# Optimization experiments

Hardware: AMD Instinct MI355X
Metric: run time of the kernel (lower is better)

Reference implementation:

```python
import jax, jax.numpy as jnp
import numpy as np

# ---- config (matches init_kwargs) ----
M, N, D = 8, 512, 243            # meshes, neurons per mesh, input dim
E_RATIO = 0.8
NE = int(N * E_RATIO)            # 409 excitatory
NI = N - NE                      # 103 inhibitory
TICKS = 16
BATCH = 512
BITS = 4
WSCALE = 8.0
VTH, VRESET = 1.0, 0.0
TAU_E, TAU_I, DT = 2.0, 1.5, 1.0
BETA = 10.0                      # fast-sigmoid surrogate slope
INPUT_SCALE = 1.0


def fake_quant(w):
    """Quantization-aware fake quant with straight-through estimator."""
    step = WSCALE / (2 ** (BITS - 1))          # 1.0 for 4-bit, scale 8
    q = jnp.clip(jnp.round(w / step), -(2 ** (BITS - 1)), 2 ** (BITS - 1) - 1) * step
    return w + jax.lax.stop_gradient(q - w)


@jax.custom_vjp
def spike(u):
    return (u >= 0.0).astype(u.dtype)

def _spike_fwd(u):
    return spike(u), u

def _spike_bwd(u, g):
    # fast-sigmoid surrogate gradient
    return (g * BETA / (1.0 + BETA * jnp.abs(u)) ** 2,)

spike.defvjp(_spike_fwd, _spike_bwd)


def setup_inputs() -> dict:
    key = jax.random.key(0)
    ks = jax.random.split(key, 8)

    def sparse_w(k, shape, density, std, zero_diag=False):
        km, kw = jax.random.split(k)
        mask = (jax.random.uniform(km, shape) < density).astype(jnp.float32)
        if zero_diag:
            mask = mask * (1.0 - jnp.eye(shape[-1], dtype=jnp.float32))
        return jax.random.normal(kw, shape) * std * mask

    x = jax.random.normal(ks[0], (BATCH, D), dtype=jnp.float32)
    W_in = jax.random.normal(ks[1], (M, N, D)) * 0.8      # per-mesh input projection [out,in]
    b_in = jax.random.normal(ks[2], (M, N)) * 0.05
    W_inter = sparse_w(ks[3], (M, N, NE), 0.3, 0.8)        # inter-mesh: E of mesh m -> mesh m+1
    W_EE = sparse_w(ks[4], (M, NE, NE), 0.5, 0.8, True)
    W_EI = sparse_w(ks[5], (M, NI, NE), 0.6, 0.8)
    W_IE = sparse_w(ks[6], (M, NE, NI), 0.8, 0.8)
    W_II = sparse_w(ks[7], (M, NI, NI), 0.7, 0.8, True)
    return dict(x=x, W_in=W_in, b_in=b_in, W_inter=W_inter,
                W_EE=W_EE, W_EI=W_EI, W_IE=W_IE, W_II=W_II)


def reference(x, W_in, b_in, W_inter, W_EE, W_EI, W_IE, W_II):
    B = x.shape[0]
    decay_E = 1.0 - DT / TAU_E
    decay_I = 1.0 - DT / TAU_I

    # quantize weights once (constant across ticks)
    qW_in, qW_inter = fake_quant(W_in), fake_quant(W_inter)
    qW_EE, qW_EI = fake_quant(W_EE), fake_quant(W_EI)
    qW_IE, qW_II = fake_quant(W_IE), fake_quant(W_II)

    # external input projection, same every tick: [M, B, N]
    ext_proj = jnp.einsum('bd,mnd->mbn', x * INPUT_SCALE, qW_in) + b_in[:, None, :]

    def tick(carry, _):
        e, i, vE, vI, acc = carry          # e:[M,B,NE] i:[M,B,NI]
        # inter-mesh: mesh m receives inter_connections[m-1](e_prev[m-1])
        inter = jnp.einsum('mbe,mne->mbn', e, qW_inter)
        ext = ext_proj + jnp.roll(inter, 1, axis=0)
        cE = ext[:, :, :NE] \
            + jnp.einsum('mbe,mfe->mbf', e, qW_EE) \
            + jnp.einsum('mbi,mfi->mbf', i, qW_IE)
        cI = ext[:, :, NE:] \
            + jnp.einsum('mbe,mfe->mbf', e, qW_EI) \
            + jnp.einsum('mbi,mfi->mbf', i, qW_II)
        # LIF: leaky decay + input, threshold, hard reset
        vE = vE * decay_E + cE * DT
        vI = vI * decay_I + cI * DT
        sE = spike(vE - VTH)
        sI = spike(vI - VTH)
        vE = sE * VRESET + (1.0 - sE) * vE
        vI = sI * VRESET + (1.0 - sI) * vI
        acc = acc + jnp.concatenate([sE, sI], axis=-1)
        return (sE, sI, vE, vI, acc), None

    z = jnp.zeros
    carry0 = (z((M, B, NE)), z((M, B, NI)), z((M, B, NE)), z((M, B, NI)), z((M, B, N)))
    (eF, iF, vEF, vIF, acc), _ = jax.lax.scan(tick, carry0, None, length=TICKS)
    # accumulator laid out mesh-major: [B, M*N]
    return jnp.transpose(acc, (1, 0, 2)).reshape(B, M * N)
```

## Files before the change

kernel.cpp:

```cpp
#include <hip/hip_runtime.h>
#include <hip/hip_bf16.h>

#define Mm 8
#define Nn 512
#define NEe 409
#define NIi 103
#define Bb 512
#define Dd 243
#define Tt 16
#define SPB 96
#define SPTICK (Mm * Bb * SPB)
#define WCROW 1152
#define DEC_I 0.33333334f
#define NBLK 256
#define FLAGSTRIDE 16
#define SPINMAX 1000000L
#define ABROW 176
#define ZSPAN_U32 1581056

typedef int v4i __attribute__((ext_vector_type(4)));

__device__ __forceinline__ float quantf(float w) {
    float q = rintf(w);
    return fminf(fmaxf(q, -8.0f), 7.0f);
}

__device__ __forceinline__ v4i unpack16(unsigned int dl, unsigned int dh, bool qhi, int qsh) {
    unsigned int d = qhi ? dh : dl;
    v4i r;
    r[0] = (int)((((d >> qsh) & 0xFu) * 0x00204081u) & 0x01010101u);
    r[1] = (int)((((d >> (qsh + 4)) & 0xFu) * 0x00204081u) & 0x01010101u);
    r[2] = (int)((((d >> (qsh + 8)) & 0xFu) * 0x00204081u) & 0x01010101u);
    r[3] = (int)((((d >> (qsh + 12)) & 0xFu) * 0x00204081u) & 0x01010101u);
    return r;
}

__global__ void k_pack(const float* __restrict__ Wint, const float* __restrict__ WEE,
                       const float* __restrict__ WEI, const float* __restrict__ WIE,
                       const float* __restrict__ WII, signed char* __restrict__ Wc,
                       unsigned* __restrict__ spz) {
    int gid = blockIdx.x * 256 + threadIdx.x;
#pragma unroll
    for (int z = 0; z < 2; ++z) {
        int i = gid + z * 1179648;
        if (i < ZSPAN_U32) spz[i] = 0u;
    }
    int q = gid;
    if (q >= (Mm * Nn * WCROW) / 4) return;
    int k0 = (q * 4) % WCROW;
    int n  = ((q * 4) / WCROW) & (Nn - 1);
    int m  = (q * 4) / (WCROW * Nn);
    char out4[4];
#pragma unroll
    for (int j = 0; j < 4; ++j) {
        int k = k0 + j;
        float w = 0.0f;
        if (k < 512) {
            if (k < NEe) w = Wint[((((m + 7) & 7) * Nn) + n) * NEe + k];
        } else if (k < 1024) {
            int jj = k - 512;
            if (jj < NEe) w = (n < NEe) ? WEE[((m * NEe) + n) * NEe + jj]
                                        : WEI[((m * NIi) + (n - NEe)) * NEe + jj];
        } else {
            int jj = k - 1049;
            if (jj >= 0 && jj < NIi) w = (n < NEe) ? WIE[((m * NEe) + n) * NIi + jj]
                                        : WII[((m * NIi) + (n - NEe)) * NIi + jj];
        }
        out4[j] = (signed char)(int)quantf(w);
    }
    *(int*)&Wc[q * 4] = *(int*)out4;
}

__global__ void __launch_bounds__(512, 2)
k_ticks(const signed char* __restrict__ Wc,
        unsigned char* __restrict__ Sp,
        const float* __restrict__ x,
        const float* __restrict__ Win,
        const float* __restrict__ bin,
        float* __restrict__ out,
        int* __restrict__ flags) {
    __shared__ __align__(16) signed char sB[128 * WCROW];
    __shared__ __align__(16) unsigned char sAb[64 * ABROW];

    const int wg = blockIdx.x;
    const int m  = wg & 7;
    const int bt = (wg >> 3) & 7;
    const int nt = wg >> 6;
    const int b0 = bt * 64;
    const int n0 = nt * 128;
    const int pm = (m + 7) & 7;

    const int tid  = threadIdx.x;
    const int w    = tid >> 6;
    const int lane = tid & 63;
    const int bh   = w & 1;
    const int nh   = w >> 1;
    const int quad = lane >> 4;
    const int li   = lane & 15;

    int waitIdx = 0;
    if (tid < 8) {
        int mm = (tid < 4) ? pm : m;
        waitIdx = (((tid & 3) << 6) | (bt << 3) | mm) * FLAGSTRIDE;
    }

    float decs[2]; int nels[2];
    int styp[2], soff[2];
#pragma unroll
    for (int tn = 0; tn < 2; ++tn) {
        int n = n0 + nh * 32 + tn * 16 + li;
        nels[tn] = n;
        decs[tn] = (n < NEe) ? 0.5f : DEC_I;
        int nb = n0 + nh * 32 + tn * 16;
        if (nb < 400)      { styp[tn] = 0; soff[tn] = nb >> 3; }
        else if (nb == 400){ styp[tn] = 2; soff[tn] = 50; }
        else               { styp[tn] = 1; soff[tn] = 64 + ((nb - 384) >> 3); }
    }
    const int bbase = b0 + bh * 32;

    {
        const int g   = tid >> 8;
        const int t8  = tid & 255;
        const int n0e = n0 + g * 64;
        float* xs  = (float*)sB + g * (2 * 64 * 68);
        float* wsm = xs + 64 * 68;
        const int etb4 = (t8 & 15) * 4;
        const int etn4 = (t8 >> 4) * 4;
        const int sr = t8 >> 2;
        const int sc = (t8 & 3) * 16;
        float c[4][4];
#pragma unroll
        for (int i = 0; i < 4; ++i)
#pragma unroll
            for (int j = 0; j < 4; ++j) c[i][j] = 0.0f;

        for (int d0 = 0; d0 < Dd; d0 += 64) {
#pragma unroll
            for (int j = 0; j < 16; ++j) {
                int d = d0 + sc + j;
                float xv = 0.0f, wv = 0.0f;
                if (d < Dd) {
                    xv = x[(b0 + sr) * Dd + d];
                    wv = quantf(Win[((m * Nn) + n0e + sr) * Dd + d]);
                }
                xs[(sc + j) * 68 + sr] = xv;
                wsm[(sc + j) * 68 + sr] = wv;
            }
            __syncthreads();
            const int dmax = min(64, Dd - d0);
            for (int d = 0; d < dmax; ++d) {
                float4 av = *(const float4*)&xs[d * 68 + etb4];
                float4 wv = *(const float4*)&wsm[d * 68 + etn4];
                float a[4] = {av.x, av.y, av.z, av.w};
                float wq[4] = {wv.x, wv.y, wv.z, wv.w};
#pragma unroll
                for (int i = 0; i < 4; ++i)
#pragma unroll
                    for (int j = 0; j < 4; ++j)
                        c[i][j] = fmaf(a[i], wq[j], c[i][j]);
            }
            __syncthreads();
        }
        float* extbuf = (float*)sB;
#pragma unroll
        for (int i = 0; i < 4; ++i)
#pragma unroll
            for (int j = 0; j < 4; ++j)
                extbuf[(etb4 + i) * 128 + g * 64 + etn4 + j] =
                    __fadd_rn(c[i][j], bin[m * Nn + n0e + etn4 + j]);
        __syncthreads();
    }

    float extr[2][2][4];
#pragma unroll
    for (int tb = 0; tb < 2; ++tb)
#pragma unroll
        for (int tn = 0; tn < 2; ++tn)
#pragma unroll
            for (int r = 0; r < 4; ++r)
                extr[tb][tn][r] = ((const float*)sB)[(bh * 32 + tb * 16 + quad * 4 + r) * 128
                                                     + (nels[tn] - n0)];
    __syncthreads();

    const signed char* WcBase = Wc + (size_t)(m * Nn + n0) * WCROW;
#pragma unroll
    for (int j = 0; j < 18; ++j) {
        int task = tid + j * 512;
        int row = task / 72, gg = task % 72;
        v4i v = *(const v4i*)(WcBase + (size_t)row * WCROW + gg * 16);
        int gs = (gg < 64) ? ((gg & 48) | ((gg ^ row) & 15))
                           : (64 + ((gg ^ row) & 7));
        *(v4i*)&sB[row * WCROW + gs * 16] = v;
    }
    if (tid < 384) {
        int row = tid / 6, z = tid - (tid / 6) * 6;
        int s = (z < 3) ? (13 + z) : (26 + z);
        *(unsigned*)&sAb[row * ABROW + s * 4] = 0u;
    }
    __syncthreads();

    float vmem[2][2][4];
    int cnt[2][2];
#pragma unroll
    for (int tb = 0; tb < 2; ++tb)
#pragma unroll
        for (int tn = 0; tn < 2; ++tn) {
            cnt[tb][tn] = 0;
#pragma unroll
            for (int r = 0; r < 4; ++r) vmem[tb][tn][r] = 0.0f;
        }

    const bool qhi = (quad >= 2);
    const int qsh = (quad & 1) << 4;
    const int r0base = (bh * 32 + li) * ABROW;
    const int r1base = (bh * 32 + 16 + li) * ABROW;

    for (int t = 0; t < Tt; ++t) {
        float c[2][2][4];

        if (t == 0) {
#pragma unroll
            for (int tb = 0; tb < 2; ++tb)
#pragma unroll
                for (int tn = 0; tn < 2; ++tn)
#pragma unroll
                    for (int r = 0; r < 4; ++r)
                        c[tb][tn][r] = __fadd_rn(__fadd_rn(__fadd_rn(extr[tb][tn][r], 0.0f), 0.0f), 0.0f);
        } else {
            if (tid < 8) {
                long spin = 0;
                while (__hip_atomic_load(&flags[waitIdx],
                                         __ATOMIC_RELAXED, __HIP_MEMORY_SCOPE_AGENT) < t) {
                    __builtin_amdgcn_s_sleep(2);
                    if (++spin > SPINMAX) break;
                }
            }
            __syncthreads();

            const unsigned char* SR = Sp + (size_t)(t - 1) * SPTICK;
            const unsigned char* PrevRow = SR + (size_t)(pm * Bb + b0) * SPB;
            const unsigned char* OwnRow  = SR + (size_t)(m  * Bb + b0) * SPB;
#pragma unroll
            for (int j = 0; j < 3; ++j) {
                int task = tid + j * 512;
                if (task < 1152) {
                    int row = task / 18, s = task % 18;
                    const unsigned char* src;
                    int dstoff;
                    if (s < 8)       { src = PrevRow + (size_t)row * SPB + s * 8;            dstoff = s * 8; }
                    else if (s < 16) { src = OwnRow  + (size_t)row * SPB + (s - 8) * 8;      dstoff = s * 8; }
                    else             { src = OwnRow  + (size_t)row * SPB + 64 + (s - 16) * 8; dstoff = 128 + (s - 16) * 8; }
                    unsigned long long vb = __hip_atomic_load((const unsigned long long*)src,
                                               __ATOMIC_RELAXED, __HIP_MEMORY_SCOPE_AGENT);
                    *(unsigned long long*)&sAb[row * ABROW + dstoff] = vb;
                }
            }
            __syncthreads();

            v4i acc[2][2];
#pragma unroll
            for (int tb = 0; tb < 2; ++tb)
#pragma unroll
                for (int tn = 0; tn < 2; ++tn) acc[tb][tn] = (v4i){0, 0, 0, 0};

#pragma unroll
            for (int ch = 0; ch < 4; ++ch) {
                const int cb = ch << 8;
                v4i a0lo = *(const v4i*)&sAb[r0base + (cb >> 3)];
                v4i a0hi = *(const v4i*)&sAb[r0base + (cb >> 3) + 16];
                v4i a1lo = *(const v4i*)&sAb[r1base + (cb >> 3)];
                v4i a1hi = *(const v4i*)&sAb[r1base + (cb >> 3) + 16];
#pragma unroll
                for (int ks = 0; ks < 256; ks += 64) {
                    v4i s0 = (ks < 128) ? a0lo : a0hi;
                    v4i s1 = (ks < 128) ? a1lo : a1hi;
                    const int D0 = ((ks >> 6) & 1) ? 2 : 0;
                    v4i af0 = unpack16((unsigned int)s0[D0], (unsigned int)s0[D0 + 1], qhi, qsh);
                    v4i af1 = unpack16((unsigned int)s1[D0], (unsigned int)s1[D0 + 1], qhi, qsh);
                    const int gs = (cb >> 4) + ((((ks >> 4) + quad) ^ li) & 15);
#pragma unroll
                    for (int tn = 0; tn < 2; ++tn) {
                        const v4i bfr = *(const v4i*)&sB[(nh * 32 + tn * 16 + li) * WCROW + gs * 16];
                        acc[0][tn] = __builtin_amdgcn_mfma_i32_16x16x64_i8(af0, bfr, acc[0][tn], 0, 0, 0);
                        acc[1][tn] = __builtin_amdgcn_mfma_i32_16x16x64_i8(af1, bfr, acc[1][tn], 0, 0, 0);
                    }
                }
                if (ch == 1) {
#pragma unroll
                    for (int tb = 0; tb < 2; ++tb)
#pragma unroll
                        for (int tn = 0; tn < 2; ++tn) {
#pragma unroll
                            for (int r = 0; r < 4; ++r)
                                c[tb][tn][r] = __fadd_rn(extr[tb][tn][r], (float)acc[tb][tn][r]);
                            acc[tb][tn] = (v4i){0, 0, 0, 0};
                        }
                } else if (ch == 3) {
#pragma unroll
                    for (int tb = 0; tb < 2; ++tb)
#pragma unroll
                        for (int tn = 0; tn < 2; ++tn) {
#pragma unroll
                            for (int r = 0; r < 4; ++r)
                                c[tb][tn][r] = __fadd_rn(c[tb][tn][r], (float)acc[tb][tn][r]);
                            acc[tb][tn] = (v4i){0, 0, 0, 0};
                        }
                }
            }
            {
                v4i e0 = *(const v4i*)&sAb[r0base + 128];
                v4i e1 = *(const v4i*)&sAb[r1base + 128];
#pragma unroll
                for (int ks = 0; ks < 128; ks += 64) {
                    const int D0 = (ks >> 6) ? 2 : 0;
                    v4i af0 = unpack16((unsigned int)e0[D0], (unsigned int)e0[D0 + 1], qhi, qsh);
                    v4i af1 = unpack16((unsigned int)e1[D0], (unsigned int)e1[D0 + 1], qhi, qsh);
                    const int gs = 64 + ((((ks >> 4) + quad) ^ li) & 7);
#pragma unroll
                    for (int tn = 0; tn < 2; ++tn) {
                        const v4i bfr = *(const v4i*)&sB[(nh * 32 + tn * 16 + li) * WCROW + gs * 16];
                        acc[0][tn] = __builtin_amdgcn_mfma_i32_16x16x64_i8(af0, bfr, acc[0][tn], 0, 0, 0);
                        acc[1][tn] = __builtin_amdgcn_mfma_i32_16x16x64_i8(af1, bfr, acc[1][tn], 0, 0, 0);
                    }
                }
            }
#pragma unroll
            for (int tb = 0; tb < 2; ++tb)
#pragma unroll
                for (int tn = 0; tn < 2; ++tn)
#pragma unroll
                    for (int r = 0; r < 4; ++r)
                        c[tb][tn][r] = __fadd_rn(c[tb][tn][r], (float)acc[tb][tn][r]);
        }

        int snow[2][2] = {{0, 0}, {0, 0}};
#pragma unroll
        for (int tb = 0; tb < 2; ++tb)
#pragma unroll
            for (int tn = 0; tn < 2; ++tn)
#pragma unroll
                for (int r = 0; r < 4; ++r) {
                    float vn = __fadd_rn(__fmul_rn(vmem[tb][tn][r], decs[tn]), c[tb][tn][r]);
                    int s = (vn >= 1.0f) ? 1 : 0;
                    vmem[tb][tn][r] = s ? 0.0f : vn;
                    cnt[tb][tn] += s << (r * 8);
                    snow[tb][tn] |= s << r;
                }

        if (t < Tt - 1) {
            unsigned char* SW = Sp + (size_t)t * SPTICK;
#pragma unroll
            for (int tb = 0; tb < 2; ++tb)
#pragma unroll
                for (int tn = 0; tn < 2; ++tn)
#pragma unroll
                    for (int r = 0; r < 4; ++r) {
                        unsigned long long mk = __ballot((snow[tb][tn] >> r) & 1);
                        if (li == 0) {
                            unsigned short v = (unsigned short)(mk >> (unsigned)(quad << 4));
                            int row = bbase + tb * 16 + quad * 4 + r;
                            unsigned char* rb = SW + (size_t)(m * Bb + row) * SPB;
                            if (styp[tn] != 2) {
                                __hip_atomic_store((unsigned short*)(rb + soff[tn]), v,
                                                   __ATOMIC_RELAXED, __HIP_MEMORY_SCOPE_AGENT);
                            } else {
                                __hip_atomic_store((unsigned short*)(rb + 50),
                                                   (unsigned short)(v & 0x01FF),
                                                   __ATOMIC_RELAXED, __HIP_MEMORY_SCOPE_AGENT);
                                __hip_atomic_store((unsigned short*)(rb + 66),
                                                   (unsigned short)(v & 0xFE00),
                                                   __ATOMIC_RELAXED, __HIP_MEMORY_SCOPE_AGENT);
                            }
                        }
                    }
            __syncthreads();
            if (tid == 0)
                __hip_atomic_store(&flags[wg * FLAGSTRIDE], t + 1,
                                   __ATOMIC_RELAXED, __HIP_MEMORY_SCOPE_AGENT);
        }
    }

#pragma unroll
    for (int tb = 0; tb < 2; ++tb)
#pragma unroll
        for (int tn = 0; tn < 2; ++tn)
#pragma unroll
            for (int r = 0; r < 4; ++r) {
                int b = bbase + tb * 16 + quad * 4 + r;
                out[(size_t)b * (Mm * Nn) + m * Nn + nels[tn]] =
                    (float)((cnt[tb][tn] >> (r * 8)) & 0xff);
            }
}

extern "C" void kernel_launch(void* const* d_in, const int* in_sizes, int n_in,
                              void* d_out, int out_size, void* d_ws, size_t ws_size,
                              hipStream_t stream) {
    const float* x    = (const float*)d_in[0];
    const float* Win  = (const float*)d_in[1];
    const float* bin  = (const float*)d_in[2];
    const float* Wint = (const float*)d_in[3];
    const float* WEE  = (const float*)d_in[4];
    const float* WEI  = (const float*)d_in[5];
    const float* WIE  = (const float*)d_in[6];
    const float* WII  = (const float*)d_in[7];
    float* out = (float*)d_out;

    char* ws = (char*)d_ws;
    signed char* Wc   = (signed char*)ws;
    unsigned char* Sp = (unsigned char*)(ws + 4718592);
    int* flags = (int*)(ws + 4718592 + 16 * SPTICK);

    k_pack<<<(Mm * Nn * WCROW / 4 + 255) / 256, 256, 0, stream>>>(Wint, WEE, WEI, WIE, WII, Wc,
                                                                  (unsigned*)Sp);
    k_ticks<<<NBLK, 512, 0, stream>>>(Wc, Sp, x, Win, bin, out, flags);
}
```

Baseline: 197.0 us.

## Halve neuron tile per block and stream weights through double-buffered LDS per tick

Workgroups now cover 64 neurons instead of 128, which doubles the grid to 512 blocks of 256 threads. The full weight slab is no longer kept resident in LDS. Each tick it is streamed from global memory in 256-column chunks through a double-buffered LDS stage, so LDS use drops enough to raise occupancy and spread the recurrent work over more blocks. The cost is that weights are re-read from global/L2 on every tick, there are extra barriers per chunk, and each block now waits on twice as many inter-block flags in the persistent spin-wait scheme.

```diff
diff --git a/kernel.cpp b/kernel.cpp
--- a/kernel.cpp
+++ b/kernel.cpp
@@ -12,7 +12,7 @@
 #define SPTICK (Mm * Bb * SPB)
 #define WCROW 1152
 #define DEC_I 0.33333334f
-#define NBLK 256
+#define NBLK 512
 #define FLAGSTRIDE 16
 #define SPINMAX 1000000L
 #define ABROW 176
@@ -71,7 +71,7 @@
     *(int*)&Wc[q * 4] = *(int*)out4;
 }
 
-__global__ void __launch_bounds__(512, 2)
+__global__ void __launch_bounds__(256, 2)
 k_ticks(const signed char* __restrict__ Wc,
         unsigned char* __restrict__ Sp,
         const float* __restrict__ x,
@@ -79,15 +79,16 @@
         const float* __restrict__ bin,
         float* __restrict__ out,
         int* __restrict__ flags) {
-    __shared__ __align__(16) signed char sB[128 * WCROW];
-    __shared__ __align__(16) unsigned char sAb[64 * ABROW];
+    __shared__ __align__(16) char arena[44032];
+    signed char (*sBst)[64][256] = (signed char (*)[64][256])arena;
+    unsigned char* sAb = (unsigned char*)(arena + 32768);
 
     const int wg = blockIdx.x;
     const int m  = wg & 7;
     const int bt = (wg >> 3) & 7;
     const int nt = wg >> 6;
     const int b0 = bt * 64;
-    const int n0 = nt * 128;
+    const int n0 = nt * 64;
     const int pm = (m + 7) & 7;
 
     const int tid  = threadIdx.x;
@@ -99,9 +100,9 @@
     const int li   = lane & 15;
 
     int waitIdx = 0;
-    if (tid < 8) {
-        int mm = (tid < 4) ? pm : m;
-        waitIdx = (((tid & 3) << 6) | (bt << 3) | mm) * FLAGSTRIDE;
+    if (tid < 16) {
+        int mm = (tid < 8) ? pm : m;
+        waitIdx = (((tid & 7) << 6) | (bt << 3) | mm) * FLAGSTRIDE;
     }
 
     float decs[2]; int nels[2];
@@ -119,11 +120,9 @@
     const int bbase = b0 + bh * 32;
 
     {
-        const int g   = tid >> 8;
-        const int t8  = tid & 255;
-        const int n0e = n0 + g * 64;
-        float* xs  = (float*)sB + g * (2 * 64 * 68);
-        float* wsm = xs + 64 * 68;
+        float* xs  = (float*)arena;
+        float* wsm = (float*)arena + 64 * 68;
+        const int t8 = tid;
         const int etb4 = (t8 & 15) * 4;
         const int etn4 = (t8 >> 4) * 4;
         const int sr = t8 >> 2;
@@ -141,7 +140,7 @@
                 float xv = 0.0f, wv = 0.0f;
                 if (d < Dd) {
                     xv = x[(b0 + sr) * Dd + d];
-                    wv = quantf(Win[((m * Nn) + n0e + sr) * Dd + d]);
+                    wv = quantf(Win[((m * Nn) + n0 + sr) * Dd + d]);
                 }
                 xs[(sc + j) * 68 + sr] = xv;
                 wsm[(sc + j) * 68 + sr] = wv;
@@ -161,13 +160,13 @@
             }
             __syncthreads();
         }
-        float* extbuf = (float*)sB;
+        float* extbuf = (float*)arena;
 #pragma unroll
         for (int i = 0; i < 4; ++i)
 #pragma unroll
             for (int j = 0; j < 4; ++j)
-                extbuf[(etb4 + i) * 128 + g * 64 + etn4 + j] =
-                    __fadd_rn(c[i][j], bin[m * Nn + n0e + etn4 + j]);
+                extbuf[(etb4 + i) * 64 + etn4 + j] =
+                    __fadd_rn(c[i][j], bin[m * Nn + n0 + etn4 + j]);
         __syncthreads();
     }
 
@@ -178,26 +177,27 @@
         for (int tn = 0; tn < 2; ++tn)
 #pragma unroll
             for (int r = 0; r < 4; ++r)
-                extr[tb][tn][r] = ((const float*)sB)[(bh * 32 + tb * 16 + quad * 4 + r) * 128
-                                                     + (nels[tn] - n0)];
+                extr[tb][tn][r] = ((const float*)arena)[(bh * 32 + tb * 16 + quad * 4 + r) * 64
+                                                        + (nels[tn] - n0)];
     __syncthreads();
 
-    const signed char* WcBase = Wc + (size_t)(m * Nn + n0) * WCROW;
-#pragma unroll
-    for (int j = 0; j < 18; ++j) {
-        int task = tid + j * 512;
-        int row = task / 72, gg = task % 72;
-        v4i v = *(const v4i*)(WcBase + (size_t)row * WCROW + gg * 16);
-        int gs = (gg < 64) ? ((gg & 48) | ((gg ^ row) & 15))
-                           : (64 + ((gg ^ row) & 7));
-        *(v4i*)&sB[row * WCROW + gs * 16] = v;
-    }
-    if (tid < 384) {
-        int row = tid / 6, z = tid - (tid / 6) * 6;
+    for (int idx = tid; idx < 384; idx += 256) {
+        int row = idx / 6, z = idx - (idx / 6) * 6;
         int s = (z < 3) ? (13 + z) : (26 + z);
         *(unsigned*)&sAb[row * ABROW + s * 4] = 0u;
     }
     __syncthreads();
+
+    int rowB[4], gcolB[4], scolB[4];
+#pragma unroll
+    for (int j = 0; j < 4; ++j) {
+        int ch = tid + j * 256;
+        rowB[j]  = ch >> 4;
+        int cnk  = ch & 15;
+        gcolB[j] = cnk * 16;
+        scolB[j] = (cnk ^ (rowB[j] & 15)) * 16;
+    }
+    const signed char* WcBase = Wc + (size_t)(m * Nn + n0) * WCROW;
 
     float vmem[2][2][4];
     int cnt[2][2];
@@ -214,6 +214,7 @@
     const int qsh = (quad & 1) << 4;
     const int r0base = (bh * 32 + li) * ABROW;
     const int r1base = (bh * 32 + 16 + li) * ABROW;
+    const int bRow0 = nh * 32 + li;
 
     for (int t = 0; t < Tt; ++t) {
         float c[2][2][4];
@@ -227,7 +228,7 @@
                     for (int r = 0; r < 4; ++r)
                         c[tb][tn][r] = __fadd_rn(__fadd_rn(__fadd_rn(extr[tb][tn][r], 0.0f), 0.0f), 0.0f);
         } else {
-            if (tid < 8) {
+            if (tid < 16) {
                 long spin = 0;
                 while (__hip_atomic_load(&flags[waitIdx],
                                          __ATOMIC_RELAXED, __HIP_MEMORY_SCOPE_AGENT) < t) {
@@ -241,8 +242,8 @@
             const unsigned char* PrevRow = SR + (size_t)(pm * Bb + b0) * SPB;
             const unsigned char* OwnRow  = SR + (size_t)(m  * Bb + b0) * SPB;
 #pragma unroll
-            for (int j = 0; j < 3; ++j) {
-                int task = tid + j * 512;
+            for (int j = 0; j < 5; ++j) {
+                int task = tid + j * 256;
                 if (task < 1152) {
                     int row = task / 18, s = task % 18;
                     const unsigned char* src;
@@ -255,6 +256,10 @@
                     *(unsigned long long*)&sAb[row * ABROW + dstoff] = vb;
                 }
             }
+#pragma unroll
+            for (int j = 0; j < 4; ++j)
+                *(v4i*)&sBst[0][rowB[j]][scolB[j]] =
+                    *(const v4i*)(WcBase + (size_t)rowB[j] * WCROW + gcolB[j]);
             __syncthreads();
 
             v4i acc[2][2];
@@ -263,9 +268,18 @@
 #pragma unroll
                 for (int tn = 0; tn < 2; ++tn) acc[tb][tn] = (v4i){0, 0, 0, 0};
 
-#pragma unroll
-            for (int ch = 0; ch < 4; ++ch) {
-                const int cb = ch << 8;
+            for (int it = 0; it < 4; ++it) {
+                const int buf = it & 1;
+                const int k0 = (it + 1) * 256;
+                const int kw = (it == 3) ? 128 : 256;
+                v4i nB[4]; bool ldB[4];
+#pragma unroll
+                for (int j = 0; j < 4; ++j) {
+                    ldB[j] = (gcolB[j] < kw);
+                    if (ldB[j])
+                        nB[j] = *(const v4i*)(WcBase + (size_t)rowB[j] * WCROW + k0 + gcolB[j]);
+                }
+                const int cb = it << 8;
                 v4i a0lo = *(const v4i*)&sAb[r0base + (cb >> 3)];
                 v4i a0hi = *(const v4i*)&sAb[r0base + (cb >> 3) + 16];
                 v4i a1lo = *(const v4i*)&sAb[r1base + (cb >> 3)];
@@ -277,15 +291,20 @@
                     const int D0 = ((ks >> 6) & 1) ? 2 : 0;
                     v4i af0 = unpack16((unsigned int)s0[D0], (unsigned int)s0[D0 + 1], qhi, qsh);
                     v4i af1 = unpack16((unsigned int)s1[D0], (unsigned int)s1[D0 + 1], qhi, qsh);
-                    const int gs = (cb >> 4) + ((((ks >> 4) + quad) ^ li) & 15);
+                    const int col = ((((ks >> 4) + quad) ^ li) & 15) * 16;
 #pragma unroll
                     for (int tn = 0; tn < 2; ++tn) {
-                        const v4i bfr = *(const v4i*)&sB[(nh * 32 + tn * 16 + li) * WCROW + gs * 16];
+                        const v4i bfr = *(const v4i*)&sBst[buf][bRow0 + tn * 16][col];
                         acc[0][tn] = __builtin_amdgcn_mfma_i32_16x16x64_i8(af0, bfr, acc[0][tn], 0, 0, 0);
                         acc[1][tn] = __builtin_amdgcn_mfma_i32_16x16x64_i8(af1, bfr, acc[1][tn], 0, 0, 0);
                     }
                 }
-                if (ch == 1) {
+                const int nb2 = buf ^ 1;
+#pragma unroll
+                for (int j = 0; j < 4; ++j)
+                    if (ldB[j]) *(v4i*)&sBst[nb2][rowB[j]][scolB[j]] = nB[j];
+                __syncthreads();
+                if (it == 1) {
 #pragma unroll
                     for (int tb = 0; tb < 2; ++tb)
 #pragma unroll
@@ -295,7 +314,7 @@
                                 c[tb][tn][r] = __fadd_rn(extr[tb][tn][r], (float)acc[tb][tn][r]);
                             acc[tb][tn] = (v4i){0, 0, 0, 0};
                         }
-                } else if (ch == 3) {
+                } else if (it == 3) {
 #pragma unroll
                     for (int tb = 0; tb < 2; ++tb)
 #pragma unroll
@@ -315,10 +334,10 @@
                     const int D0 = (ks >> 6) ? 2 : 0;
                     v4i af0 = unpack16((unsigned int)e0[D0], (unsigned int)e0[D0 + 1], qhi, qsh);
                     v4i af1 = unpack16((unsigned int)e1[D0], (unsigned int)e1[D0 + 1], qhi, qsh);
-                    const int gs = 64 + ((((ks >> 4) + quad) ^ li) & 7);
+                    const int col = ((((ks >> 4) + quad)) ^ li) * 16;
 #pragma unroll
                     for (int tn = 0; tn < 2; ++tn) {
-                        const v4i bfr = *(const v4i*)&sB[(nh * 32 + tn * 16 + li) * WCROW + gs * 16];
+                        const v4i bfr = *(const v4i*)&sBst[0][bRow0 + tn * 16][col];
                         acc[0][tn] = __builtin_amdgcn_mfma_i32_16x16x64_i8(af0, bfr, acc[0][tn], 0, 0, 0);
                         acc[1][tn] = __builtin_amdgcn_mfma_i32_16x16x64_i8(af1, bfr, acc[1][tn], 0, 0, 0);
                     }
@@ -412,5 +431,5 @@
 
     k_pack<<<(Mm * Nn * WCROW / 4 + 255) / 256, 256, 0, stream>>>(Wint, WEE, WEI, WIE, WII, Wc,
                                                                   (unsigned*)Sp);
-    k_ticks<<<NBLK, 512, 0, stream>>>(Wc, Sp, x, Win, bin, out, flags);
+    k_ticks<<<NBLK, 256, 0, stream>>>(Wc, Sp, x, Win, bin, out, flags);
 }
```

Result: slower. 229.1 us (+16.3%).
